# Kernel optimization log

Measured on AMD Instinct MI355X. Metric: run time of the kernel, lower is better.

Reference implementation:

```python
import jax, jax.numpy as jnp
import numpy as np

N, E = 10000, 320000
D, H, C = 256, 8, 32   # dim, heads, head_dim (dim//num_head)
DE, DF = 64, 1024      # edge_dim, dim_ff


def setup_inputs() -> dict:
    key = jax.random.key(0)
    ks = jax.random.split(key, 32)
    s = 0.05
    n = lambda k, shp: jax.random.normal(k, shp, jnp.float32) * s
    inp = {
        "nf": jax.random.normal(ks[0], (N, D), jnp.float32),
        "ei": jax.random.randint(ks[1], (2, E), 0, N),
        "ew": jax.random.normal(ks[2], (E, DE), jnp.float32),
        # GATConv 1
        "lin1": n(ks[3], (D, H * C)), "le1": n(ks[4], (DE, H * C)),
        "asrc1": n(ks[5], (H, C)), "adst1": n(ks[6], (H, C)), "aedge1": n(ks[7], (H, C)),
        "b1": jnp.zeros((H * C,), jnp.float32),
        # GATConv 2
        "lin2": n(ks[8], (D, H * C)), "le2": n(ks[9], (DE, H * C)),
        "asrc2": n(ks[10], (H, C)), "adst2": n(ks[11], (H, C)), "aedge2": n(ks[12], (H, C)),
        "b2": jnp.zeros((H * C,), jnp.float32),
        # LayerNorms
        "g1": jnp.ones((D,), jnp.float32), "be1": jnp.zeros((D,), jnp.float32),
        "g2": jnp.ones((D,), jnp.float32), "be2": jnp.zeros((D,), jnp.float32),
        "g3": jnp.ones((D,), jnp.float32), "be3": jnp.zeros((D,), jnp.float32),
        # FFN
        "w1": n(ks[13], (D, DF)), "fb1": jnp.zeros((DF,), jnp.float32),
        "w2": n(ks[14], (DF, D)), "fb2": jnp.zeros((D,), jnp.float32),
    }
    return inp


def _ln(x, g, b, eps=1e-6):
    # annotated-transformer LayerNorm: unbiased std, eps added to std
    mu = x.mean(-1, keepdims=True)
    sd = jnp.std(x, axis=-1, ddof=1, keepdims=True)
    return g * (x - mu) / (sd + eps) + b


def _gat(x, src, dst, ea, W, We, a_s, a_d, a_e, bias):
    # PyG GATConv with edge_dim, add_self_loops=True, fill_value='mean', concat=True
    ones = jnp.ones((src.shape[0], 1), x.dtype)
    cnt = jax.ops.segment_sum(ones, dst, num_segments=N)
    loop_attr = jax.ops.segment_sum(ea, dst, num_segments=N) / jnp.maximum(cnt, 1.0)
    idx = jnp.arange(N)
    srcf = jnp.concatenate([src, idx])
    dstf = jnp.concatenate([dst, idx])
    eaf = jnp.concatenate([ea, loop_attr], axis=0)          # [E+N, DE]
    xs = (x @ W).reshape(N, H, C)                            # [N,H,C]
    ef = (eaf @ We).reshape(-1, H, C)                        # [E+N,H,C]
    a_src = (xs * a_s).sum(-1)                               # [N,H]
    a_dst = (xs * a_d).sum(-1)                               # [N,H]
    alpha = a_src[srcf] + a_dst[dstf] + (ef * a_e).sum(-1)   # [E+N,H]
    alpha = jax.nn.leaky_relu(alpha, 0.2)
    m = jax.ops.segment_max(alpha, dstf, num_segments=N)     # segment softmax
    ex = jnp.exp(alpha - m[dstf])
    den = jax.ops.segment_sum(ex, dstf, num_segments=N)
    w = ex / (den[dstf] + 1e-16)                             # [E+N,H]
    out = jax.ops.segment_sum(w[:, :, None] * xs[srcf], dstf, num_segments=N)
    return out.reshape(N, H * C) + bias


def reference(nf, ei, ew, lin1, le1, asrc1, adst1, aedge1, b1,
              lin2, le2, asrc2, adst2, aedge2, b2,
              g1, be1, g2, be2, g3, be3, w1, fb1, w2, fb2):
    src, dst = ei[0], ei[1]
    h = _gat(nf, src, dst, ew, lin1, le1, asrc1, adst1, aedge1, b1)
    nf = nf + jax.nn.leaky_relu(_ln(h, g1, be1), 0.01)
    h = _gat(nf, src, dst, ew, lin2, le2, asrc2, adst2, aedge2, b2)
    nf = nf + jax.nn.leaky_relu(_ln(h, g2, be2), 0.01)
    h = jax.nn.relu(nf @ w1 + fb1) @ w2 + fb2
    nf = nf + jax.nn.leaky_relu(_ln(h, g3, be3), 0.01)
    return nf
```

## Files before the change

### kernel.cpp

```cpp
#include <hip/hip_runtime.h>
#include <hip/hip_bf16.h>
#include <math.h>

#define D 256
#define H 8
#define C 32
#define DE 64
#define DF 1024

static inline size_t align_up(size_t x, size_t a) { return (x + a - 1) / a * a; }

typedef __attribute__((ext_vector_type(8))) short short8;
typedef __attribute__((ext_vector_type(4))) float f32x4;

__device__ inline unsigned short f2b(float x) {
    __hip_bfloat16 h = __float2bfloat16(x);
    return *reinterpret_cast<unsigned short*>(&h);
}
__device__ inline float b2f(unsigned short u) {
    return __uint_as_float(((unsigned int)u) << 16);
}

__global__ void deg_kernel(const int* __restrict__ dst, int* __restrict__ deg, int E) {
    int e = blockIdx.x * 256 + threadIdx.x;
    if (e < E) atomicAdd(&deg[dst[e]], 1);
}

__global__ void partial_sum_kernel(const int* __restrict__ deg, int* __restrict__ part, int n) {
    int i = blockIdx.x * 256 + threadIdx.x;
    int v = (i < n) ? deg[i] : 0;
    for (int o = 1; o < 64; o <<= 1) v += __shfl_xor(v, o);
    __shared__ int w4[4];
    if ((threadIdx.x & 63) == 0) w4[threadIdx.x >> 6] = v;
    __syncthreads();
    if (threadIdx.x == 0) part[blockIdx.x] = w4[0] + w4[1] + w4[2] + w4[3];
}

__global__ void scan_part_kernel(int* __restrict__ part, int nb) {
    __shared__ int buf[256];
    int t = threadIdx.x;
    buf[t] = (t < nb) ? part[t] : 0;
    __syncthreads();
    for (int s = 1; s < 256; s <<= 1) {
        int v = (t >= s) ? buf[t - s] : 0;
        __syncthreads();
        buf[t] += v;
        __syncthreads();
    }
    int excl = (t == 0) ? 0 : buf[t - 1];
    if (t < nb) part[t] = excl;
}

__global__ void scan_final_kernel(const int* __restrict__ deg, const int* __restrict__ part,
                                  int* __restrict__ off, int n) {
    int b = blockIdx.x, t = threadIdx.x, i = b * 256 + t;
    __shared__ int buf[256];
    int v = (i < n) ? deg[i] : 0;
    buf[t] = v;
    __syncthreads();
    for (int s = 1; s < 256; s <<= 1) {
        int x = (t >= s) ? buf[t - s] : 0;
        __syncthreads();
        buf[t] += x;
        __syncthreads();
    }
    int excl = part[b] + buf[t] - v;
    if (i < n) off[i] = excl;
    if (i == n - 1) off[n] = excl + v;
}

__global__ void copy_int_kernel(const int* __restrict__ a, int* __restrict__ b, int n) {
    int i = blockIdx.x * 256 + threadIdx.x;
    if (i < n) b[i] = a[i];
}

__global__ void fill_kernel(const int* __restrict__ src, const int* __restrict__ dst,
                            int* __restrict__ cursor, int* __restrict__ eid,
                            int* __restrict__ src_csr, int E) {
    int e = blockIdx.x * 256 + threadIdx.x;
    if (e < E) {
        int p = atomicAdd(&cursor[dst[e]], 1);
        eid[p] = e;
        src_csr[p] = src[e];
    }
}

__global__ void convert_bf16x8_kernel(const float* __restrict__ in, unsigned short* __restrict__ out,
                                      size_t n_valid, size_t n_total) {
    size_t i = ((size_t)blockIdx.x * 256 + threadIdx.x) * 8;
    if (i >= n_total) return;
    ushort4 o0, o1;
    if (i < n_valid) {
        float4 a = *(const float4*)&in[i];
        float4 b = *(const float4*)&in[i + 4];
        o0.x = f2b(a.x); o0.y = f2b(a.y); o0.z = f2b(a.z); o0.w = f2b(a.w);
        o1.x = f2b(b.x); o1.y = f2b(b.y); o1.z = f2b(b.z); o1.w = f2b(b.w);
    } else {
        o0.x = o0.y = o0.z = o0.w = 0;
        o1 = o0;
    }
    *(ushort4*)&out[i] = o0;
    *(ushort4*)&out[i + 4] = o1;
}

__global__ void transpose_bf16_kernel(const float* __restrict__ in, unsigned short* __restrict__ out,
                                      int K, int N) {
    __shared__ float tile[32][33];
    int bn = blockIdx.x * 32, bk = blockIdx.y * 32;
    int tx = threadIdx.x & 31, ty = threadIdx.x >> 5;
    for (int i = ty; i < 32; i += 8) {
        int k = bk + i, n = bn + tx;
        tile[i][tx] = (k < K && n < N) ? in[(size_t)k * N + n] : 0.f;
    }
    __syncthreads();
    for (int i = ty; i < 32; i += 8) {
        int n = bn + i, k = bk + tx;
        if (n < N && k < K) out[(size_t)n * K + k] = f2b(tile[tx][i]);
    }
}

__global__ __launch_bounds__(256) void mfma_gemm_kernel(
    const unsigned short* __restrict__ A, const unsigned short* __restrict__ BT,
    const float* __restrict__ bias, float* __restrict__ Cf, unsigned short* __restrict__ Cb,
    int M, int Nc, int K, int relu) {
    __shared__ unsigned short As[128 * 64];
    __shared__ unsigned short Bs[128 * 64];
    int t = threadIdx.x;
    int lane = t & 63, w = t >> 6;
    int gm0 = blockIdx.x * 128, gn0 = blockIdx.y * 128;
    f32x4 acc[4][4] = {};
    int srow = lane >> 3, scol = (lane & 7) * 8;
    int wm = (w >> 1) * 64, wn = (w & 1) * 64;
    int fr = lane & 15, fk = (lane >> 4) * 8;

    for (int k0 = 0; k0 < K; k0 += 64) {
        __syncthreads();
#pragma unroll
        for (int i = 0; i < 4; ++i) {
            int rb = w * 32 + i * 8;
            const unsigned short* ga = A + (size_t)(gm0 + rb + srow) * K + k0 + scol;
            __builtin_amdgcn_global_load_lds(
                (const __attribute__((address_space(1))) unsigned int*)ga,
                (__attribute__((address_space(3))) unsigned int*)&As[rb * 64], 16, 0, 0);
            const unsigned short* gb = BT + (size_t)(gn0 + rb + srow) * K + k0 + scol;
            __builtin_amdgcn_global_load_lds(
                (const __attribute__((address_space(1))) unsigned int*)gb,
                (__attribute__((address_space(3))) unsigned int*)&Bs[rb * 64], 16, 0, 0);
        }
        __syncthreads();
#pragma unroll
        for (int kk = 0; kk < 64; kk += 32) {
            short8 a[4], b[4];
#pragma unroll
            for (int m = 0; m < 4; ++m)
                a[m] = *(const short8*)&As[(wm + m * 16 + fr) * 64 + kk + fk];
#pragma unroll
            for (int n = 0; n < 4; ++n)
                b[n] = *(const short8*)&Bs[(wn + n * 16 + fr) * 64 + kk + fk];
#pragma unroll
            for (int m = 0; m < 4; ++m)
#pragma unroll
                for (int n = 0; n < 4; ++n)
                    acc[m][n] = __builtin_amdgcn_mfma_f32_16x16x32_bf16(a[m], b[n], acc[m][n], 0, 0, 0);
        }
    }
    int fcol = lane & 15, frow4 = (lane >> 4) * 4;
#pragma unroll
    for (int m = 0; m < 4; ++m) {
#pragma unroll
        for (int i = 0; i < 4; ++i) {
            int gr = gm0 + wm + m * 16 + frow4 + i;
            if (gr >= M) continue;
#pragma unroll
            for (int n = 0; n < 4; ++n) {
                int gc = gn0 + wn + n * 16 + fcol;
                float v = acc[m][n][i];
                if (bias) v += bias[gc];
                if (relu) v = fmaxf(v, 0.f);
                if (Cb) Cb[(size_t)gr * Nc + gc] = f2b(v);
                else    Cf[(size_t)gr * Nc + gc] = v;
            }
        }
    }
}

__global__ void me_kernel(const float* __restrict__ We, const float* __restrict__ ae,
                          float* __restrict__ Me) {
    int t = threadIdx.x;
    int d = t >> 3, h = t & 7;
    float s = 0.f;
    for (int c = 0; c < C; ++c) s += We[d * (H * C) + h * C + c] * ae[h * C + c];
    Me[d * H + h] = s;
}

__global__ void ealpha_csr_kernel(const float* __restrict__ ew, const int* __restrict__ eid,
                                  const float* __restrict__ Me1, const float* __restrict__ Me2,
                                  float* __restrict__ eA1c, float* __restrict__ eA2c, int E) {
    __shared__ float M1[DE * H], M2[DE * H];
    int t = threadIdx.x;
    for (int i = t; i < DE * H; i += 256) { M1[i] = Me1[i]; M2[i] = Me2[i]; }
    __syncthreads();
    int p = blockIdx.x * 256 + t;
    if (p >= E) return;
    int e = eid[p];
    const float* row = ew + (size_t)e * DE;
    float a1[8] = {}, a2[8] = {};
#pragma unroll
    for (int i = 0; i < 16; ++i) {
        float4 rv = *(const float4*)&row[i * 4];
#pragma unroll
        for (int j = 0; j < 4; ++j) {
            float v = ((const float*)&rv)[j];
            int d = i * 4 + j;
#pragma unroll
            for (int hh = 0; hh < 8; ++hh) {
                a1[hh] = fmaf(v, M1[d * 8 + hh], a1[hh]);
                a2[hh] = fmaf(v, M2[d * 8 + hh], a2[hh]);
            }
        }
    }
#pragma unroll
    for (int hh = 0; hh < 8; ++hh) {
        eA1c[(size_t)p * 8 + hh] = a1[hh];
        eA2c[(size_t)p * 8 + hh] = a2[hh];
    }
}

__global__ void attnparam_kernel(const unsigned short* __restrict__ xsb,
                                 const float* __restrict__ a_s, const float* __restrict__ a_d,
                                 float* __restrict__ asrc, float* __restrict__ adst, int N) {
    __shared__ float AS[D], AD[D];
    int t = threadIdx.x;
    AS[t] = a_s[t]; AD[t] = a_d[t];
    __syncthreads();
    int idx = blockIdx.x * 256 + t;
    int n = idx >> 3, hh = idx & 7;
    if (n < N) {
        const unsigned short* rowp = xsb + (size_t)n * D + hh * C;
        float s1 = 0.f, s2 = 0.f;
#pragma unroll
        for (int i = 0; i < 8; ++i) {
            ushort4 u = *(const ushort4*)&rowp[i * 4];
            float v0 = b2f(u.x), v1 = b2f(u.y), v2 = b2f(u.z), v3 = b2f(u.w);
            s1 += v0 * AS[hh * C + i * 4] + v1 * AS[hh * C + i * 4 + 1] +
                  v2 * AS[hh * C + i * 4 + 2] + v3 * AS[hh * C + i * 4 + 3];
            s2 += v0 * AD[hh * C + i * 4] + v1 * AD[hh * C + i * 4 + 1] +
                  v2 * AD[hh * C + i * 4 + 2] + v3 * AD[hh * C + i * 4 + 3];
        }
        asrc[idx] = s1; adst[idx] = s2;
    }
}

__global__ __launch_bounds__(256) void gat_node_kernel(
    const int* __restrict__ off, const int* __restrict__ src_csr,
    const float* __restrict__ eAc,
    const float* __restrict__ asrc, const float* __restrict__ adst,
    const unsigned short* __restrict__ xsb, const float* __restrict__ nf_in,
    const float* __restrict__ bias, const float* __restrict__ gamma,
    const float* __restrict__ beta, float* __restrict__ nf_out,
    unsigned short* __restrict__ nf_out_b, int N) {
    int lane = threadIdx.x & 63;
    int n = blockIdx.x * 4 + (threadIdx.x >> 6);
    if (n >= N) return;
    int e0 = off[n], e1 = off[n + 1], deg = e1 - e0;
    int h = lane & 7;
    int hw = lane >> 3;

    float adstn = adst[n * 8 + h];

    float acc0 = 0.f, acc1 = 0.f, acc2 = 0.f, acc3 = 0.f;
    float den0 = 0.f, easum = 0.f;
    int nfull = deg >> 3, rem = deg & 7;
    int p = e0 + hw;
    for (int it = 0; it < nfull; ++it, p += 8) {
        int s = src_csr[p];
        float ea = eAc[(size_t)p * 8 + h];
        float al = asrc[s * 8 + h] + adstn + ea;
        al = al > 0.f ? al : 0.2f * al;
        float ex = expf(al);
        den0 += ex;
        easum += ea;
#pragma unroll
        for (int kk = 0; kk < 8; ++kk) {
            int sl = kk * 8 + hw;
            float exk = __shfl(ex, sl);
            int sk = __shfl(s, sl);
            ushort4 u = *(const ushort4*)&xsb[(size_t)sk * D + lane * 4];
            acc0 = fmaf(exk, b2f(u.x), acc0);
            acc1 = fmaf(exk, b2f(u.y), acc1);
            acc2 = fmaf(exk, b2f(u.z), acc2);
            acc3 = fmaf(exk, b2f(u.w), acc3);
        }
    }
    if (rem) {
        float ex = 0.f; int s = 0;
        if (hw < rem) {
            s = src_csr[p];
            float ea = eAc[(size_t)p * 8 + h];
            float al = asrc[s * 8 + h] + adstn + ea;
            al = al > 0.f ? al : 0.2f * al;
            ex = expf(al);
            den0 += ex;
            easum += ea;
        }
        for (int kk = 0; kk < rem; ++kk) {
            int sl = kk * 8 + hw;
            float exk = __shfl(ex, sl);
            int sk = __shfl(s, sl);
            ushort4 u = *(const ushort4*)&xsb[(size_t)sk * D + lane * 4];
            acc0 = fmaf(exk, b2f(u.x), acc0);
            acc1 = fmaf(exk, b2f(u.y), acc1);
            acc2 = fmaf(exk, b2f(u.z), acc2);
            acc3 = fmaf(exk, b2f(u.w), acc3);
        }
    }
    den0  += __shfl_xor(den0, 8);
    den0  += __shfl_xor(den0, 16);
    den0  += __shfl_xor(den0, 32);
    easum += __shfl_xor(easum, 8);
    easum += __shfl_xor(easum, 16);
    easum += __shfl_xor(easum, 32);
    float sa = easum / (float)(deg > 0 ? deg : 1);
    float als = asrc[n * 8 + h] + adstn + sa;
    als = als > 0.f ? als : 0.2f * als;
    float exSelf = expf(als);
    {
        float exs = __shfl(exSelf, hw);
        ushort4 u = *(const ushort4*)&xsb[(size_t)n * D + lane * 4];
        acc0 = fmaf(exs, b2f(u.x), acc0);
        acc1 = fmaf(exs, b2f(u.y), acc1);
        acc2 = fmaf(exs, b2f(u.z), acc2);
        acc3 = fmaf(exs, b2f(u.w), acc3);
    }
    den0 += exSelf;
    float denOwn = __shfl(den0, hw);
    float inv = 1.f / (denOwn + 1e-16f);

    int t0 = lane * 4;
    float4 bi = *(const float4*)&bias[t0];
    float o0 = acc0 * inv + bi.x;
    float o1 = acc1 * inv + bi.y;
    float o2 = acc2 * inv + bi.z;
    float o3 = acc3 * inv + bi.w;

    float s1 = o0 + o1 + o2 + o3;
    float s2 = o0 * o0 + o1 * o1 + o2 * o2 + o3 * o3;
    for (int o = 1; o < 64; o <<= 1) { s1 += __shfl_xor(s1, o); s2 += __shfl_xor(s2, o); }
    float mu = s1 / 256.f;
    float var = fmaxf((s2 - 256.f * mu * mu) / 255.f, 0.f);
    float sdv = sqrtf(var) + 1e-6f;
    float4 ga = *(const float4*)&gamma[t0];
    float4 be = *(const float4*)&beta[t0];
    float4 nin = *(const float4*)&nf_in[(size_t)n * D + t0];
    float y0 = ga.x * (o0 - mu) / sdv + be.x; y0 = y0 > 0.f ? y0 : 0.01f * y0;
    float y1 = ga.y * (o1 - mu) / sdv + be.y; y1 = y1 > 0.f ? y1 : 0.01f * y1;
    float y2 = ga.z * (o2 - mu) / sdv + be.z; y2 = y2 > 0.f ? y2 : 0.01f * y2;
    float y3 = ga.w * (o3 - mu) / sdv + be.w; y3 = y3 > 0.f ? y3 : 0.01f * y3;
    float r0 = nin.x + y0, r1 = nin.y + y1, r2 = nin.z + y2, r3 = nin.w + y3;
    float4 outv; outv.x = r0; outv.y = r1; outv.z = r2; outv.w = r3;
    *(float4*)&nf_out[(size_t)n * D + t0] = outv;
    ushort4 ob; ob.x = f2b(r0); ob.y = f2b(r1); ob.z = f2b(r2); ob.w = f2b(r3);
    *(ushort4*)&nf_out_b[(size_t)n * D + t0] = ob;
}

__global__ void ln_residual_kernel(const float* __restrict__ hin, const float* __restrict__ nf_in,
                                   const float* __restrict__ gamma, const float* __restrict__ beta,
                                   float* __restrict__ out) {
    int n = blockIdx.x, t = threadIdx.x;
    float v = hin[(size_t)n * D + t];
    float s1 = v, s2 = v * v;
    for (int o = 1; o < 64; o <<= 1) { s1 += __shfl_xor(s1, o); s2 += __shfl_xor(s2, o); }
    __shared__ float r1[4], r2[4];
    int w = t >> 6;
    if ((t & 63) == 0) { r1[w] = s1; r2[w] = s2; }
    __syncthreads();
    float tot1 = r1[0] + r1[1] + r1[2] + r1[3];
    float tot2 = r2[0] + r2[1] + r2[2] + r2[3];
    float mu = tot1 / (float)D;
    float var = fmaxf((tot2 - (float)D * mu * mu) / (float)(D - 1), 0.f);
    float sd = sqrtf(var) + 1e-6f;
    float y = gamma[t] * (v - mu) / sd + beta[t];
    y = y > 0.f ? y : 0.01f * y;
    out[(size_t)n * D + t] = nf_in[(size_t)n * D + t] + y;
}

extern "C" void kernel_launch(void* const* d_in, const int* in_sizes, int n_in,
                              void* d_out, int out_size, void* d_ws, size_t ws_size,
                              hipStream_t stream) {
    const float* nf0    = (const float*)d_in[0];
    const int*   ei     = (const int*)d_in[1];
    const float* ew     = (const float*)d_in[2];
    const float* lin1   = (const float*)d_in[3];
    const float* le1    = (const float*)d_in[4];
    const float* asrc1w = (const float*)d_in[5];
    const float* adst1w = (const float*)d_in[6];
    const float* aedge1 = (const float*)d_in[7];
    const float* b1     = (const float*)d_in[8];
    const float* lin2   = (const float*)d_in[9];
    const float* le2    = (const float*)d_in[10];
    const float* asrc2w = (const float*)d_in[11];
    const float* adst2w = (const float*)d_in[12];
    const float* aedge2 = (const float*)d_in[13];
    const float* b2     = (const float*)d_in[14];
    const float* g1     = (const float*)d_in[15];
    const float* be1    = (const float*)d_in[16];
    const float* g2     = (const float*)d_in[17];
    const float* be2    = (const float*)d_in[18];
    const float* g3     = (const float*)d_in[19];
    const float* be3    = (const float*)d_in[20];
    const float* w1     = (const float*)d_in[21];
    const float* fb1    = (const float*)d_in[22];
    const float* w2     = (const float*)d_in[23];
    const float* fb2    = (const float*)d_in[24];

    const int N = in_sizes[0] / D;
    const int E = in_sizes[1] / 2;
    const int Mpad = ((N + 127) / 128) * 128;
    const int* srcI = ei;
    const int* dstI = ei + E;

    char* ws = (char*)d_ws;
    size_t ob = 0;
    auto alloc = [&](size_t bytes) { void* p = ws + ob; ob = align_up(ob + bytes, 256); return p; };
    int*   deg     = (int*)alloc((size_t)N * 4);
    int*   csr_off = (int*)alloc((size_t)(N + 1) * 4);
    int*   cursor  = (int*)alloc((size_t)N * 4);
    int*   part    = (int*)alloc(1024);
    int*   eid     = (int*)alloc((size_t)E * 4);
    int*   src_csr = (int*)alloc((size_t)E * 4);
    float* Me1     = (float*)alloc(DE * H * 4);
    float* Me2     = (float*)alloc(DE * H * 4);
    float* asrcB   = (float*)alloc((size_t)N * H * 4);
    float* adstB   = (float*)alloc((size_t)N * H * 4);
    float* eA1c    = (float*)alloc((size_t)E * H * 4);
    float* eA2c    = (float*)alloc((size_t)E * H * 4);
    float* xsf     = (float*)alloc((size_t)Mpad * D * 4);
    float* nfw     = (float*)alloc((size_t)N * D * 4);
    unsigned short* xs_b  = (unsigned short*)alloc((size_t)Mpad * D * 2);
    unsigned short* Abf   = (unsigned short*)alloc((size_t)Mpad * D * 2);
    unsigned short* lin1T = (unsigned short*)alloc((size_t)D * D * 2);
    unsigned short* lin2T = (unsigned short*)alloc((size_t)D * D * 2);
    unsigned short* w1T   = (unsigned short*)alloc((size_t)DF * D * 2);
    unsigned short* w2T   = (unsigned short*)alloc((size_t)D * DF * 2);
    unsigned short* hidden = (unsigned short*)ws;
    (void)ws_size;
    float* out = (float*)d_out;

    hipMemsetAsync(deg, 0, (size_t)N * 4, stream);

    int eb = (E + 255) / 256;
    int nb = (N + 255) / 256;
    deg_kernel<<<eb, 256, 0, stream>>>(dstI, deg, E);
    partial_sum_kernel<<<nb, 256, 0, stream>>>(deg, part, N);
    scan_part_kernel<<<1, 256, 0, stream>>>(part, nb);
    scan_final_kernel<<<nb, 256, 0, stream>>>(deg, part, csr_off, N);
    copy_int_kernel<<<nb, 256, 0, stream>>>(csr_off, cursor, N);
    fill_kernel<<<eb, 256, 0, stream>>>(srcI, dstI, cursor, eid, src_csr, E);

    me_kernel<<<1, 512, 0, stream>>>(le1, aedge1, Me1);
    me_kernel<<<1, 512, 0, stream>>>(le2, aedge2, Me2);
    ealpha_csr_kernel<<<eb, 256, 0, stream>>>(ew, eid, Me1, Me2, eA1c, eA2c, E);

    transpose_bf16_kernel<<<dim3(D / 32, D / 32), 256, 0, stream>>>(lin1, lin1T, D, D);
    transpose_bf16_kernel<<<dim3(D / 32, D / 32), 256, 0, stream>>>(lin2, lin2T, D, D);
    transpose_bf16_kernel<<<dim3(DF / 32, D / 32), 256, 0, stream>>>(w1, w1T, D, DF);
    transpose_bf16_kernel<<<dim3(D / 32, DF / 32), 256, 0, stream>>>(w2, w2T, DF, D);

    const size_t nvalid = (size_t)N * D, ntot = (size_t)Mpad * D;
    int cb = (int)((ntot / 8 + 255) / 256);
    int gatb = (N + 3) / 4;

    convert_bf16x8_kernel<<<cb, 256, 0, stream>>>(nf0, Abf, nvalid, ntot);
    mfma_gemm_kernel<<<dim3(Mpad / 128, D / 128), 256, 0, stream>>>(
        Abf, lin1T, nullptr, nullptr, xs_b, N, D, D, 0);
    attnparam_kernel<<<(N * H + 255) / 256, 256, 0, stream>>>(xs_b, asrc1w, adst1w, asrcB, adstB, N);
    gat_node_kernel<<<gatb, 256, 0, stream>>>(csr_off, src_csr, eA1c, asrcB, adstB,
                                              xs_b, nf0, b1, g1, be1, nfw, Abf, N);
    mfma_gemm_kernel<<<dim3(Mpad / 128, D / 128), 256, 0, stream>>>(
        Abf, lin2T, nullptr, nullptr, xs_b, N, D, D, 0);
    attnparam_kernel<<<(N * H + 255) / 256, 256, 0, stream>>>(xs_b, asrc2w, adst2w, asrcB, adstB, N);
    gat_node_kernel<<<gatb, 256, 0, stream>>>(csr_off, src_csr, eA2c, asrcB, adstB,
                                              xs_b, nfw, b2, g2, be2, nfw, Abf, N);
    mfma_gemm_kernel<<<dim3(Mpad / 128, DF / 128), 256, 0, stream>>>(
        Abf, w1T, fb1, nullptr, hidden, N, DF, D, 1);
    mfma_gemm_kernel<<<dim3(Mpad / 128, D / 128), 256, 0, stream>>>(
        hidden, w2T, fb2, xsf, nullptr, N, D, DF, 0);
    ln_residual_kernel<<<N, 256, 0, stream>>>(xsf, nfw, g3, be3, out);
}
```

Baseline: 280.5 us.

## Fuse attention params into GEMM, MFMA edge alpha, merge setup kernels, prefetch GAT

The attention-parameter dot products are folded into the epilogue of a new 64-row GEMM tile variant, which also gives the 256-wide GEMMs more blocks. The per-edge alpha projection now runs on MFMA in edge order and is permuted to CSR order afterwards, instead of an FMA loop over scattered edge rows. The four weight transposes become one launch, the cursor copy is merged into the scan, and the GAT node loop software-prefetches the next batch of edge data. These changes cut launch count and memory traffic in exchange for an extra intermediate buffer, bf16 rounding of the edge features, and more complex control flow.

```diff
diff --git a/kernel.cpp b/kernel.cpp
--- a/kernel.cpp
+++ b/kernel.cpp
@@ -52,7 +52,7 @@
 }
 
 __global__ void scan_final_kernel(const int* __restrict__ deg, const int* __restrict__ part,
-                                  int* __restrict__ off, int n) {
+                                  int* __restrict__ off, int* __restrict__ cursor, int n) {
     int b = blockIdx.x, t = threadIdx.x, i = b * 256 + t;
     __shared__ int buf[256];
     int v = (i < n) ? deg[i] : 0;
@@ -65,13 +65,8 @@
         __syncthreads();
     }
     int excl = part[b] + buf[t] - v;
-    if (i < n) off[i] = excl;
+    if (i < n) { off[i] = excl; cursor[i] = excl; }
     if (i == n - 1) off[n] = excl + v;
-}
-
-__global__ void copy_int_kernel(const int* __restrict__ a, int* __restrict__ b, int n) {
-    int i = blockIdx.x * 256 + threadIdx.x;
-    if (i < n) b[i] = a[i];
 }
 
 __global__ void fill_kernel(const int* __restrict__ src, const int* __restrict__ dst,
@@ -103,45 +98,60 @@
     *(ushort4*)&out[i + 4] = o1;
 }
 
-__global__ void transpose_bf16_kernel(const float* __restrict__ in, unsigned short* __restrict__ out,
-                                      int K, int N) {
+__global__ void transpose4_bf16_kernel(const float* __restrict__ lin1, const float* __restrict__ lin2,
+                                       const float* __restrict__ w1, const float* __restrict__ w2,
+                                       unsigned short* __restrict__ lin1T, unsigned short* __restrict__ lin2T,
+                                       unsigned short* __restrict__ w1T, unsigned short* __restrict__ w2T) {
     __shared__ float tile[32][33];
-    int bn = blockIdx.x * 32, bk = blockIdx.y * 32;
+    int b = blockIdx.x;
+    const float* in; unsigned short* outp; int K, N, tt;
+    if (b < 64)       { in = lin1; outp = lin1T; K = D;  N = D;  tt = b; }
+    else if (b < 128) { in = lin2; outp = lin2T; K = D;  N = D;  tt = b - 64; }
+    else if (b < 384) { in = w1;   outp = w1T;   K = D;  N = DF; tt = b - 128; }
+    else              { in = w2;   outp = w2T;   K = DF; N = D;  tt = b - 384; }
+    int ntn = N >> 5;
+    int bn = (tt % ntn) * 32, bk = (tt / ntn) * 32;
     int tx = threadIdx.x & 31, ty = threadIdx.x >> 5;
-    for (int i = ty; i < 32; i += 8) {
-        int k = bk + i, n = bn + tx;
-        tile[i][tx] = (k < K && n < N) ? in[(size_t)k * N + n] : 0.f;
-    }
+    for (int i = ty; i < 32; i += 8)
+        tile[i][tx] = in[(size_t)(bk + i) * N + bn + tx];
     __syncthreads();
-    for (int i = ty; i < 32; i += 8) {
-        int n = bn + i, k = bk + tx;
-        if (n < N && k < K) out[(size_t)n * K + k] = f2b(tile[tx][i]);
-    }
-}
-
+    for (int i = ty; i < 32; i += 8)
+        outp[(size_t)(bn + i) * K + bk + tx] = f2b(tile[tx][i]);
+}
+
+template<int BM>
 __global__ __launch_bounds__(256) void mfma_gemm_kernel(
     const unsigned short* __restrict__ A, const unsigned short* __restrict__ BT,
     const float* __restrict__ bias, float* __restrict__ Cf, unsigned short* __restrict__ Cb,
-    int M, int Nc, int K, int relu) {
-    __shared__ unsigned short As[128 * 64];
+    int M, int Nc, int K, int relu,
+    const float* __restrict__ a_s, const float* __restrict__ a_d,
+    float* __restrict__ asrcO, float* __restrict__ adstO) {
+    constexpr int NR = (BM == 128) ? 4 : 2;
+    constexpr int AI = BM / 32;
+    __shared__ unsigned short As[BM * 64];
     __shared__ unsigned short Bs[128 * 64];
     int t = threadIdx.x;
     int lane = t & 63, w = t >> 6;
-    int gm0 = blockIdx.x * 128, gn0 = blockIdx.y * 128;
-    f32x4 acc[4][4] = {};
+    int gm0 = blockIdx.x * BM, gn0 = blockIdx.y * 128;
+    f32x4 acc[4][NR] = {};
     int srow = lane >> 3, scol = (lane & 7) * 8;
-    int wm = (w >> 1) * 64, wn = (w & 1) * 64;
+    int wm = (BM == 128) ? (w >> 1) * 64 : 0;
+    int wn = (BM == 128) ? (w & 1) * 64 : w * 32;
     int fr = lane & 15, fk = (lane >> 4) * 8;
 
     for (int k0 = 0; k0 < K; k0 += 64) {
         __syncthreads();
 #pragma unroll
-        for (int i = 0; i < 4; ++i) {
-            int rb = w * 32 + i * 8;
+        for (int i = 0; i < AI; ++i) {
+            int rb = w * (8 * AI) + i * 8;
             const unsigned short* ga = A + (size_t)(gm0 + rb + srow) * K + k0 + scol;
             __builtin_amdgcn_global_load_lds(
                 (const __attribute__((address_space(1))) unsigned int*)ga,
                 (__attribute__((address_space(3))) unsigned int*)&As[rb * 64], 16, 0, 0);
+        }
+#pragma unroll
+        for (int i = 0; i < 4; ++i) {
+            int rb = w * 32 + i * 8;
             const unsigned short* gb = BT + (size_t)(gn0 + rb + srow) * K + k0 + scol;
             __builtin_amdgcn_global_load_lds(
                 (const __attribute__((address_space(1))) unsigned int*)gb,
@@ -150,17 +160,17 @@
         __syncthreads();
 #pragma unroll
         for (int kk = 0; kk < 64; kk += 32) {
-            short8 a[4], b[4];
+            short8 a[4], b[NR];
 #pragma unroll
             for (int m = 0; m < 4; ++m)
                 a[m] = *(const short8*)&As[(wm + m * 16 + fr) * 64 + kk + fk];
 #pragma unroll
-            for (int n = 0; n < 4; ++n)
+            for (int n = 0; n < NR; ++n)
                 b[n] = *(const short8*)&Bs[(wn + n * 16 + fr) * 64 + kk + fk];
 #pragma unroll
             for (int m = 0; m < 4; ++m)
 #pragma unroll
-                for (int n = 0; n < 4; ++n)
+                for (int n = 0; n < NR; ++n)
                     acc[m][n] = __builtin_amdgcn_mfma_f32_16x16x32_bf16(a[m], b[n], acc[m][n], 0, 0, 0);
         }
     }
@@ -172,7 +182,7 @@
             int gr = gm0 + wm + m * 16 + frow4 + i;
             if (gr >= M) continue;
 #pragma unroll
-            for (int n = 0; n < 4; ++n) {
+            for (int n = 0; n < NR; ++n) {
                 int gc = gn0 + wn + n * 16 + fcol;
                 float v = acc[m][n][i];
                 if (bias) v += bias[gc];
@@ -182,73 +192,86 @@
             }
         }
     }
-}
-
-__global__ void me_kernel(const float* __restrict__ We, const float* __restrict__ ae,
-                          float* __restrict__ Me) {
+    if (BM == 64 && a_s) {
+        int head = (gn0 >> 5) + w;
+        float as0 = a_s[head * 32 + fcol], as1 = a_s[head * 32 + 16 + fcol];
+        float ad0 = a_d[head * 32 + fcol], ad1 = a_d[head * 32 + 16 + fcol];
+#pragma unroll
+        for (int m = 0; m < 4; ++m) {
+#pragma unroll
+            for (int i = 0; i < 4; ++i) {
+                float vs = acc[m][0][i] * as0 + acc[m][1][i] * as1;
+                float vd = acc[m][0][i] * ad0 + acc[m][1][i] * ad1;
+#pragma unroll
+                for (int o = 1; o < 16; o <<= 1) {
+                    vs += __shfl_xor(vs, o);
+                    vd += __shfl_xor(vd, o);
+                }
+                int r = gm0 + m * 16 + frow4 + i;
+                if (fcol == 0 && r < M) {
+                    asrcO[r * 8 + head] = vs;
+                    adstO[r * 8 + head] = vd;
+                }
+            }
+        }
+    }
+}
+
+__global__ void meT_kernel(const float* __restrict__ le1, const float* __restrict__ ae1,
+                           const float* __restrict__ le2, const float* __restrict__ ae2,
+                           unsigned short* __restrict__ MeT) {
     int t = threadIdx.x;
     int d = t >> 3, h = t & 7;
-    float s = 0.f;
-    for (int c = 0; c < C; ++c) s += We[d * (H * C) + h * C + c] * ae[h * C + c];
-    Me[d * H + h] = s;
-}
-
-__global__ void ealpha_csr_kernel(const float* __restrict__ ew, const int* __restrict__ eid,
-                                  const float* __restrict__ Me1, const float* __restrict__ Me2,
+    float s1 = 0.f, s2 = 0.f;
+    for (int c = 0; c < C; ++c) {
+        s1 += le1[d * (H * C) + h * C + c] * ae1[h * C + c];
+        s2 += le2[d * (H * C) + h * C + c] * ae2[h * C + c];
+    }
+    MeT[h * 64 + d] = f2b(s1);
+    MeT[(8 + h) * 64 + d] = f2b(s2);
+}
+
+__global__ __launch_bounds__(256) void ealpha_mfma_kernel(const float* __restrict__ ew,
+                                                          const unsigned short* __restrict__ MeT,
+                                                          float* __restrict__ eAe, int E) {
+    int t = threadIdx.x;
+    int lane = t & 63, w = t >> 6;
+    int e0 = blockIdx.x * 64 + w * 16;
+    int r = lane & 15, g = lane >> 4;
+    int er = e0 + r; if (er > E - 1) er = E - 1;
+    const float* rowp = ew + (size_t)er * DE;
+    float4 x0 = *(const float4*)&rowp[g * 8];
+    float4 x1 = *(const float4*)&rowp[g * 8 + 4];
+    float4 y0 = *(const float4*)&rowp[32 + g * 8];
+    float4 y1 = *(const float4*)&rowp[32 + g * 8 + 4];
+    short8 a0, a1;
+    a0[0] = (short)f2b(x0.x); a0[1] = (short)f2b(x0.y); a0[2] = (short)f2b(x0.z); a0[3] = (short)f2b(x0.w);
+    a0[4] = (short)f2b(x1.x); a0[5] = (short)f2b(x1.y); a0[6] = (short)f2b(x1.z); a0[7] = (short)f2b(x1.w);
+    a1[0] = (short)f2b(y0.x); a1[1] = (short)f2b(y0.y); a1[2] = (short)f2b(y0.z); a1[3] = (short)f2b(y0.w);
+    a1[4] = (short)f2b(y1.x); a1[5] = (short)f2b(y1.y); a1[6] = (short)f2b(y1.z); a1[7] = (short)f2b(y1.w);
+    short8 b0 = *(const short8*)&MeT[r * 64 + g * 8];
+    short8 b1 = *(const short8*)&MeT[r * 64 + 32 + g * 8];
+    f32x4 acc = {};
+    acc = __builtin_amdgcn_mfma_f32_16x16x32_bf16(a0, b0, acc, 0, 0, 0);
+    acc = __builtin_amdgcn_mfma_f32_16x16x32_bf16(a1, b1, acc, 0, 0, 0);
+#pragma unroll
+    for (int i = 0; i < 4; ++i) {
+        int ee = e0 + g * 4 + i;
+        if (ee < E) eAe[(size_t)ee * 16 + r] = acc[i];
+    }
+}
+
+__global__ void permute_ea_kernel(const float* __restrict__ eAe, const int* __restrict__ eid,
                                   float* __restrict__ eA1c, float* __restrict__ eA2c, int E) {
-    __shared__ float M1[DE * H], M2[DE * H];
-    int t = threadIdx.x;
-    for (int i = t; i < DE * H; i += 256) { M1[i] = Me1[i]; M2[i] = Me2[i]; }
-    __syncthreads();
-    int p = blockIdx.x * 256 + t;
+    int p = blockIdx.x * 256 + threadIdx.x;
     if (p >= E) return;
     int e = eid[p];
-    const float* row = ew + (size_t)e * DE;
-    float a1[8] = {}, a2[8] = {};
-#pragma unroll
-    for (int i = 0; i < 16; ++i) {
-        float4 rv = *(const float4*)&row[i * 4];
-#pragma unroll
-        for (int j = 0; j < 4; ++j) {
-            float v = ((const float*)&rv)[j];
-            int d = i * 4 + j;
-#pragma unroll
-            for (int hh = 0; hh < 8; ++hh) {
-                a1[hh] = fmaf(v, M1[d * 8 + hh], a1[hh]);
-                a2[hh] = fmaf(v, M2[d * 8 + hh], a2[hh]);
-            }
-        }
-    }
-#pragma unroll
-    for (int hh = 0; hh < 8; ++hh) {
-        eA1c[(size_t)p * 8 + hh] = a1[hh];
-        eA2c[(size_t)p * 8 + hh] = a2[hh];
-    }
-}
-
-__global__ void attnparam_kernel(const unsigned short* __restrict__ xsb,
-                                 const float* __restrict__ a_s, const float* __restrict__ a_d,
-                                 float* __restrict__ asrc, float* __restrict__ adst, int N) {
-    __shared__ float AS[D], AD[D];
-    int t = threadIdx.x;
-    AS[t] = a_s[t]; AD[t] = a_d[t];
-    __syncthreads();
-    int idx = blockIdx.x * 256 + t;
-    int n = idx >> 3, hh = idx & 7;
-    if (n < N) {
-        const unsigned short* rowp = xsb + (size_t)n * D + hh * C;
-        float s1 = 0.f, s2 = 0.f;
-#pragma unroll
-        for (int i = 0; i < 8; ++i) {
-            ushort4 u = *(const ushort4*)&rowp[i * 4];
-            float v0 = b2f(u.x), v1 = b2f(u.y), v2 = b2f(u.z), v3 = b2f(u.w);
-            s1 += v0 * AS[hh * C + i * 4] + v1 * AS[hh * C + i * 4 + 1] +
-                  v2 * AS[hh * C + i * 4 + 2] + v3 * AS[hh * C + i * 4 + 3];
-            s2 += v0 * AD[hh * C + i * 4] + v1 * AD[hh * C + i * 4 + 1] +
-                  v2 * AD[hh * C + i * 4 + 2] + v3 * AD[hh * C + i * 4 + 3];
-        }
-        asrc[idx] = s1; adst[idx] = s2;
-    }
+    const float4* src = (const float4*)&eAe[(size_t)e * 16];
+    float4 v0 = src[0], v1 = src[1], v2 = src[2], v3 = src[3];
+    float4* d1 = (float4*)&eA1c[(size_t)p * 8];
+    float4* d2 = (float4*)&eA2c[(size_t)p * 8];
+    d1[0] = v0; d1[1] = v1;
+    d2[0] = v2; d2[1] = v3;
 }
 
 __global__ __launch_bounds__(256) void gat_node_kernel(
@@ -270,49 +293,54 @@
 
     float acc0 = 0.f, acc1 = 0.f, acc2 = 0.f, acc3 = 0.f;
     float den0 = 0.f, easum = 0.f;
-    int nfull = deg >> 3, rem = deg & 7;
-    int p = e0 + hw;
-    for (int it = 0; it < nfull; ++it, p += 8) {
-        int s = src_csr[p];
-        float ea = eAc[(size_t)p * 8 + h];
-        float al = asrc[s * 8 + h] + adstn + ea;
+    int nb8 = (deg + 7) >> 3;
+
+    bool act = hw < deg;
+    int sp = e0 + hw;
+    int s_cur = act ? src_csr[sp] : n;
+    float ea_cur = act ? eAc[(size_t)sp * 8 + h] : 0.f;
+    float as_cur = act ? asrc[s_cur * 8 + h] : 0.f;
+
+    for (int it = 0; it < nb8; ++it) {
+        int base = it * 8;
+        bool actn = (base + 8 + hw) < deg;
+        int spn = e0 + base + 8 + hw;
+        int s_nx = actn ? src_csr[spn] : n;
+        float ea_nx = actn ? eAc[(size_t)spn * 8 + h] : 0.f;
+        float as_nx = actn ? asrc[s_nx * 8 + h] : 0.f;
+
+        float al = as_cur + adstn + ea_cur;
         al = al > 0.f ? al : 0.2f * al;
-        float ex = expf(al);
+        float ex = act ? expf(al) : 0.f;
         den0 += ex;
-        easum += ea;
-#pragma unroll
-        for (int kk = 0; kk < 8; ++kk) {
-            int sl = kk * 8 + hw;
-            float exk = __shfl(ex, sl);
-            int sk = __shfl(s, sl);
-            ushort4 u = *(const ushort4*)&xsb[(size_t)sk * D + lane * 4];
-            acc0 = fmaf(exk, b2f(u.x), acc0);
-            acc1 = fmaf(exk, b2f(u.y), acc1);
-            acc2 = fmaf(exk, b2f(u.z), acc2);
-            acc3 = fmaf(exk, b2f(u.w), acc3);
+        easum += ea_cur;
+
+        int lim = deg - base; if (lim > 8) lim = 8;
+        if (lim == 8) {
+#pragma unroll
+            for (int kk = 0; kk < 8; ++kk) {
+                int sl = kk * 8 + hw;
+                float exk = __shfl(ex, sl);
+                int sk = __shfl(s_cur, sl);
+                ushort4 u = *(const ushort4*)&xsb[(size_t)sk * D + lane * 4];
+                acc0 = fmaf(exk, b2f(u.x), acc0);
+                acc1 = fmaf(exk, b2f(u.y), acc1);
+                acc2 = fmaf(exk, b2f(u.z), acc2);
+                acc3 = fmaf(exk, b2f(u.w), acc3);
+            }
+        } else {
+            for (int kk = 0; kk < lim; ++kk) {
+                int sl = kk * 8 + hw;
+                float exk = __shfl(ex, sl);
+                int sk = __shfl(s_cur, sl);
+                ushort4 u = *(const ushort4*)&xsb[(size_t)sk * D + lane * 4];
+                acc0 = fmaf(exk, b2f(u.x), acc0);
+                acc1 = fmaf(exk, b2f(u.y), acc1);
+                acc2 = fmaf(exk, b2f(u.z), acc2);
+                acc3 = fmaf(exk, b2f(u.w), acc3);
+            }
         }
-    }
-    if (rem) {
-        float ex = 0.f; int s = 0;
-        if (hw < rem) {
-            s = src_csr[p];
-            float ea = eAc[(size_t)p * 8 + h];
-            float al = asrc[s * 8 + h] + adstn + ea;
-            al = al > 0.f ? al : 0.2f * al;
-            ex = expf(al);
-            den0 += ex;
-            easum += ea;
-        }
-        for (int kk = 0; kk < rem; ++kk) {
-            int sl = kk * 8 + hw;
-            float exk = __shfl(ex, sl);
-            int sk = __shfl(s, sl);
-            ushort4 u = *(const ushort4*)&xsb[(size_t)sk * D + lane * 4];
-            acc0 = fmaf(exk, b2f(u.x), acc0);
-            acc1 = fmaf(exk, b2f(u.y), acc1);
-            acc2 = fmaf(exk, b2f(u.z), acc2);
-            acc3 = fmaf(exk, b2f(u.w), acc3);
-        }
+        s_cur = s_nx; ea_cur = ea_nx; as_cur = as_nx; act = actn;
     }
     den0  += __shfl_xor(den0, 8);
     den0  += __shfl_xor(den0, 16);
@@ -428,10 +456,10 @@
     int*   part    = (int*)alloc(1024);
     int*   eid     = (int*)alloc((size_t)E * 4);
     int*   src_csr = (int*)alloc((size_t)E * 4);
-    float* Me1     = (float*)alloc(DE * H * 4);
-    float* Me2     = (float*)alloc(DE * H * 4);
+    unsigned short* MeT = (unsigned short*)alloc(16 * 64 * 2);
     float* asrcB   = (float*)alloc((size_t)N * H * 4);
     float* adstB   = (float*)alloc((size_t)N * H * 4);
+    float* eAe     = (float*)alloc((size_t)E * 16 * 4);
     float* eA1c    = (float*)alloc((size_t)E * H * 4);
     float* eA2c    = (float*)alloc((size_t)E * H * 4);
     float* xsf     = (float*)alloc((size_t)Mpad * D * 4);
@@ -453,37 +481,31 @@
     deg_kernel<<<eb, 256, 0, stream>>>(dstI, deg, E);
     partial_sum_kernel<<<nb, 256, 0, stream>>>(deg, part, N);
     scan_part_kernel<<<1, 256, 0, stream>>>(part, nb);
-    scan_final_kernel<<<nb, 256, 0, stream>>>(deg, part, csr_off, N);
-    copy_int_kernel<<<nb, 256, 0, stream>>>(csr_off, cursor, N);
+    scan_final_kernel<<<nb, 256, 0, stream>>>(deg, part, csr_off, cursor, N);
     fill_kernel<<<eb, 256, 0, stream>>>(srcI, dstI, cursor, eid, src_csr, E);
 
-    me_kernel<<<1, 512, 0, stream>>>(le1, aedge1, Me1);
-    me_kernel<<<1, 512, 0, stream>>>(le2, aedge2, Me2);
-    ealpha_csr_kernel<<<eb, 256, 0, stream>>>(ew, eid, Me1, Me2, eA1c, eA2c, E);
-
-    transpose_bf16_kernel<<<dim3(D / 32, D / 32), 256, 0, stream>>>(lin1, lin1T, D, D);
-    transpose_bf16_kernel<<<dim3(D / 32, D / 32), 256, 0, stream>>>(lin2, lin2T, D, D);
-    transpose_bf16_kernel<<<dim3(DF / 32, D / 32), 256, 0, stream>>>(w1, w1T, D, DF);
-    transpose_bf16_kernel<<<dim3(D / 32, DF / 32), 256, 0, stream>>>(w2, w2T, DF, D);
+    meT_kernel<<<1, 512, 0, stream>>>(le1, aedge1, le2, aedge2, MeT);
+    ealpha_mfma_kernel<<<(E + 63) / 64, 256, 0, stream>>>(ew, MeT, eAe, E);
+    permute_ea_kernel<<<eb, 256, 0, stream>>>(eAe, eid, eA1c, eA2c, E);
+
+    transpose4_bf16_kernel<<<640, 256, 0, stream>>>(lin1, lin2, w1, w2, lin1T, lin2T, w1T, w2T);
 
     const size_t nvalid = (size_t)N * D, ntot = (size_t)Mpad * D;
     int cb = (int)((ntot / 8 + 255) / 256);
     int gatb = (N + 3) / 4;
 
     convert_bf16x8_kernel<<<cb, 256, 0, stream>>>(nf0, Abf, nvalid, ntot);
-    mfma_gemm_kernel<<<dim3(Mpad / 128, D / 128), 256, 0, stream>>>(
-        Abf, lin1T, nullptr, nullptr, xs_b, N, D, D, 0);
-    attnparam_kernel<<<(N * H + 255) / 256, 256, 0, stream>>>(xs_b, asrc1w, adst1w, asrcB, adstB, N);
+    mfma_gemm_kernel<64><<<dim3(Mpad / 64, 2), 256, 0, stream>>>(
+        Abf, lin1T, nullptr, nullptr, xs_b, N, D, D, 0, asrc1w, adst1w, asrcB, adstB);
     gat_node_kernel<<<gatb, 256, 0, stream>>>(csr_off, src_csr, eA1c, asrcB, adstB,
                                               xs_b, nf0, b1, g1, be1, nfw, Abf, N);
-    mfma_gemm_kernel<<<dim3(Mpad / 128, D / 128), 256, 0, stream>>>(
-        Abf, lin2T, nullptr, nullptr, xs_b, N, D, D, 0);
-    attnparam_kernel<<<(N * H + 255) / 256, 256, 0, stream>>>(xs_b, asrc2w, adst2w, asrcB, adstB, N);
+    mfma_gemm_kernel<64><<<dim3(Mpad / 64, 2), 256, 0, stream>>>(
+        Abf, lin2T, nullptr, nullptr, xs_b, N, D, D, 0, asrc2w, adst2w, asrcB, adstB);
     gat_node_kernel<<<gatb, 256, 0, stream>>>(csr_off, src_csr, eA2c, asrcB, adstB,
                                               xs_b, nfw, b2, g2, be2, nfw, Abf, N);
-    mfma_gemm_kernel<<<dim3(Mpad / 128, DF / 128), 256, 0, stream>>>(
-        Abf, w1T, fb1, nullptr, hidden, N, DF, D, 1);
-    mfma_gemm_kernel<<<dim3(Mpad / 128, D / 128), 256, 0, stream>>>(
-        hidden, w2T, fb2, xsf, nullptr, N, D, DF, 0);
+    mfma_gemm_kernel<128><<<dim3(Mpad / 128, 8), 256, 0, stream>>>(
+        Abf, w1T, fb1, nullptr, hidden, N, DF, D, 1, nullptr, nullptr, nullptr, nullptr);
+    mfma_gemm_kernel<64><<<dim3(Mpad / 64, 2), 256, 0, stream>>>(
+        hidden, w2T, fb2, xsf, nullptr, N, D, DF, 0, nullptr, nullptr, nullptr, nullptr);
     ln_residual_kernel<<<N, 256, 0, stream>>>(xsf, nfw, g3, be3, out);
 }
```

Measured after the change: 263.1 us. 1.07x faster.
